# Optimization experiments

Hardware: AMD Instinct MI355X
Metric: run time of the kernel (lower is better)

Reference implementation:

```python
import jax, jax.numpy as jnp
import numpy as np

EPS = 1e-6  # nn.PairwiseDistance default eps (added to the difference)


def setup_inputs() -> dict:
    key = jax.random.key(0)
    feature = jax.random.normal(key, (16384, 256), dtype=jnp.float32)
    return {"feature": feature}


def reference(feature) -> jnp.ndarray:
    n = feature.shape[0]
    # all-pairs inner products [n, n]
    dots = jnp.matmul(feature, feature.T)
    # mask self-similarity on the diagonal with -1 (as in the torch code)
    dots = dots.at[jnp.diag_indices(n)].set(-1.0)
    # row-wise nearest neighbor (argmax of inner product)
    I = jnp.argmax(dots, axis=1)  # [n] int
    # PairwiseDistance(p=2): ||x1 - x2 + eps||_2
    diff = feature - feature[I] + EPS  # [n, d]
    distances = jnp.sqrt(jnp.sum(diff * diff, axis=1))  # [n]
    loss_uniform = -jnp.mean(jnp.log(n * distances))
    return loss_uniform
```

## Files before the change

### kernel.cpp

```cpp
#include <hip/hip_runtime.h>
#include <hip/hip_bf16.h>
#include <math.h>


#define NROWS 16384
#define DIM   256
#define BM    128
#define BN    128
#define EPSF  1e-6f

typedef __attribute__((ext_vector_type(4))) float f32x4;

typedef const __attribute__((address_space(1))) void* gas1_t;
typedef __attribute__((address_space(3))) void* las3_t;

__device__ __forceinline__ void glds16(const void* g, void* l) {
    __builtin_amdgcn_global_load_lds((gas1_t)g, (las3_t)l, 16, 0, 0);
}

__device__ __forceinline__ unsigned umax2(unsigned a, unsigned b) {
    return a > b ? a : b;
}

__device__ __forceinline__ unsigned f2e4m3(float f) {
    union { float f; unsigned u; } x; x.f = f;
    const unsigned s = (x.u >> 24) & 0x80u;
    const unsigned au = x.u & 0x7FFFFFFFu;
    float af = __uint_as_float(au);
    if (au < 0x3B800000u) {
        const int q = (int)(af * 512.0f + 0.5f);
        return s | (unsigned)q;
    }
    const unsigned add = 0x7FFFFu + ((au >> 20) & 1u);
    const unsigned v = au + add;
    const unsigned e = (v >> 23) - 120u;
    return s | (e << 3) | ((v >> 20) & 7u);
}

__global__ __launch_bounds__(256)
void convert_kernel(const float* __restrict__ F, unsigned char* __restrict__ F8,
                    unsigned long long* __restrict__ packed,
                    unsigned long long* __restrict__ scratch)
{
    const int t = blockIdx.x * 256 + threadIdx.x;
    const float4 a = *reinterpret_cast<const float4*>(F + (size_t)t * 8);
    const float4 b = *reinterpret_cast<const float4*>(F + (size_t)t * 8 + 4);
    const unsigned lo = f2e4m3(a.x) | (f2e4m3(a.y) << 8) |
                        (f2e4m3(a.z) << 16) | (f2e4m3(a.w) << 24);
    const unsigned hi = f2e4m3(b.x) | (f2e4m3(b.y) << 8) |
                        (f2e4m3(b.z) << 16) | (f2e4m3(b.w) << 24);
    uint2 v; v.x = lo; v.y = hi;
    *reinterpret_cast<uint2*>(F8 + (size_t)t * 8) = v;
    if (t < NROWS) packed[t] = 0ull;
    #pragma unroll
    for (int q = 0; q < 4; ++q)
        scratch[(size_t)t * 4 + q] = 0ull;
}

__global__ __launch_bounds__(256, 3)
void mfma_sym_fp8_kernel(const unsigned char* __restrict__ F8,
                         unsigned long long* __restrict__ packed,
                         unsigned long long* __restrict__ scratch)
{
    __shared__ __align__(16) unsigned char As[32768];
    __shared__ __align__(16) unsigned char Bs[2 * 8192];

    const int tid  = threadIdx.x;
    const int w    = tid >> 6;
    const int l    = tid & 63;
    const int rs   = (int)blockIdx.x >> 3;
    const int ck   = (int)blockIdx.x & 7;
    const int span = 128 - rs;
    const int t0   = rs + (span * ck) / 8;
    const int t1   = rs + (span * (ck + 1)) / 8;
    if (t0 >= t1) return;

    const int row0 = rs * BM;
    const int wrow = (w >> 1) * 64;
    const int wcol = (w & 1) * 64;
    const int lc   = l & 15;
    const int lr4  = l >> 4;

    #pragma unroll
    for (int m = 0; m < 8; ++m) {
        const int q   = 8 * w + m;
        const int k16 = q >> 1;
        const int row = (q & 1) * 64 + l;
        glds16(F8 + (size_t)(row0 + row) * DIM + k16 * 16, &As[q * 1024]);
    }

    #pragma unroll
    for (int q2 = 0; q2 < 2; ++q2) {
        const int col = q2 * 64 + l;
        glds16(F8 + (size_t)(t0 * BM + col) * DIM + w * 16,
               &Bs[(2 * w + q2) * 1024]);
    }

    const long* __restrict__ Al = reinterpret_cast<const long*>(As);

    f32x4 acc[4][4];
    #pragma unroll
    for (int i = 0; i < 4; ++i)
        #pragma unroll
        for (int j = 0; j < 4; ++j)
            acc[i][j] = (f32x4){512.f, 512.f, 512.f, 512.f};

    unsigned best[4][4] = {};

    const int k16r = (lr4 >> 1);
    const int odd  = lr4 & 1;

    for (int t = t0; t < t1; ++t) {
        const bool dt = (t == rs);
        #pragma unroll
        for (int ss = 0; ss < 4; ++ss) {
            __syncthreads();

            const int nt  = (ss < 3) ? t : t + 1;
            const int nss = (ss < 3) ? ss + 1 : 0;
            if (nt < t1) {
                #pragma unroll
                for (int q2 = 0; q2 < 2; ++q2) {
                    const int col = q2 * 64 + l;
                    glds16(F8 + (size_t)(nt * BM + col) * DIM + nss * 64 + w * 16,
                           &Bs[((ss & 1) ^ 1) * 8192 + (2 * w + q2) * 1024]);
                }
            }

            const long* __restrict__ Bl =
                reinterpret_cast<const long*>(Bs) + (ss & 1) * 1024;

            #pragma unroll
            for (int h = 0; h < 2; ++h) {
                const int kk = h * 2 + k16r;
                long afv[4], bfv[4];
                #pragma unroll
                for (int i = 0; i < 4; ++i) {
                    const int r = wrow + i * 16 + lc;
                    afv[i] = Al[(ss * 4 + kk) * 256 + r * 2 + odd];
                }
                #pragma unroll
                for (int j = 0; j < 4; ++j) {
                    const int c = wcol + j * 16 + lc;
                    bfv[j] = Bl[kk * 256 + c * 2 + odd];
                }
                #pragma unroll
                for (int j = 0; j < 4; ++j)
                    #pragma unroll
                    for (int i = 0; i < 4; ++i)
                        acc[i][j] = __builtin_amdgcn_mfma_f32_16x16x32_fp8_fp8(
                            afv[i], bfv[j], acc[i][j], 0, 0, 0);
            }
        }

        #pragma unroll
        for (int j = 0; j < 4; ++j) {
            unsigned kb = 0u;
            #pragma unroll
            for (int i = 0; i < 4; ++i)
                #pragma unroll
                for (int g = 0; g < 4; ++g) {
                    const int r_loc = wrow + i * 16 + lr4 * 4 + g;
                    unsigned key = (__float_as_uint(acc[i][j][g]) & 0xFFFFF800u)
                                   | (unsigned)(127 - r_loc);
                    if (dt && (wcol + j * 16 + lc == r_loc)) key = 0u;
                    kb = umax2(kb, key);
                }
            kb = umax2(kb, (unsigned)__shfl_xor((int)kb, 16));
            kb = umax2(kb, (unsigned)__shfl_xor((int)kb, 32));
            if (lr4 == 0) {
                const unsigned grow = (unsigned)row0 + (127u - (kb & 0x7FFu));
                const unsigned long long pk =
                    ((unsigned long long)(kb & 0xFFFFF800u) << 32) |
                    (0xFFFFFFFFu - grow);
                atomicMax(&scratch[((size_t)t * 128 + rs) * 128
                                   + wcol + j * 16 + lc], pk);
            }
        }

        const int tl = t - t0;
        unsigned cb[4];
        #pragma unroll
        for (int j = 0; j < 4; ++j)
            cb[j] = 2047u - (unsigned)(tl * 128 + wcol + j * 16 + lc);

        if (dt) {
            #pragma unroll
            for (int i = 0; i < 4; ++i)
                #pragma unroll
                for (int g = 0; g < 4; ++g) {
                    const int r_loc = wrow + i * 16 + lr4 * 4 + g;
                    unsigned bk = best[i][g];
                    #pragma unroll
                    for (int j = 0; j < 4; ++j) {
                        unsigned key = (__float_as_uint(acc[i][j][g])
                                        & 0xFFFFF800u) | cb[j];
                        if (wcol + j * 16 + lc == r_loc) key = 0u;
                        bk = umax2(bk, key);
                        acc[i][j][g] = 512.f;
                    }
                    best[i][g] = bk;
                }
        } else {
            #pragma unroll
            for (int i = 0; i < 4; ++i)
                #pragma unroll
                for (int g = 0; g < 4; ++g) {
                    const unsigned k0 = (__float_as_uint(acc[i][0][g]) & 0xFFFFF800u) | cb[0];
                    const unsigned k1 = (__float_as_uint(acc[i][1][g]) & 0xFFFFF800u) | cb[1];
                    const unsigned k2 = (__float_as_uint(acc[i][2][g]) & 0xFFFFF800u) | cb[2];
                    const unsigned k3 = (__float_as_uint(acc[i][3][g]) & 0xFFFFF800u) | cb[3];
                    best[i][g] = umax2(best[i][g],
                                       umax2(umax2(k0, k1), umax2(k2, k3)));
                    acc[i][0][g] = 512.f; acc[i][1][g] = 512.f;
                    acc[i][2][g] = 512.f; acc[i][3][g] = 512.f;
                }
        }
    }

    #pragma unroll
    for (int i = 0; i < 4; ++i)
        #pragma unroll
        for (int g = 0; g < 4; ++g) {
            unsigned key = best[i][g];
            #pragma unroll
            for (int m = 8; m >= 1; m >>= 1)
                key = umax2(key, (unsigned)__shfl_xor((int)key, m));
            if (lc == 0) {
                const int r = row0 + wrow + i * 16 + lr4 * 4 + g;
                const unsigned c = (unsigned)(t0 * BM) + (2047u - (key & 0x7FFu));
                const unsigned long long pk =
                    ((unsigned long long)(key & 0xFFFFF800u) << 32) |
                    (0xFFFFFFFFu - c);
                atomicMax(&packed[r], pk);
            }
        }
}

__global__ __launch_bounds__(256)
void dist_loss_kernel(const float* __restrict__ F,
                      const unsigned long long* __restrict__ packed,
                      const unsigned long long* __restrict__ scratch,
                      double* __restrict__ partials)
{
    const int tid  = threadIdx.x;
    const int lane = tid & 63;
    const int w    = tid >> 6;
    const int gw   = blockIdx.x * 4 + w;
    double local = 0.0;
    for (int r = gw; r < NROWS; r += 1024) {
        const int tR = r >> 7;
        const int cl = r & 127;
        unsigned long long best = packed[r];
        const unsigned long long* base = scratch + (size_t)tR * 16384 + cl;
        if (lane <= tR) {
            unsigned long long v = base[(size_t)lane * 128];
            if (lane + 64 <= tR) {
                const unsigned long long v2 = base[(size_t)(lane + 64) * 128];
                if (v2 > v) v = v2;
            }
            if (v > best) best = v;
        }
        #pragma unroll
        for (int m = 32; m >= 1; m >>= 1) {
            const unsigned long long o = __shfl_xor(best, m);
            if (o > best) best = o;
        }
        const int idx = (int)(0xFFFFFFFFu - (unsigned)(best & 0xFFFFFFFFull));

        const float4 a = *reinterpret_cast<const float4*>(
            F + (size_t)r * DIM + (lane << 2));
        const float4 b = *reinterpret_cast<const float4*>(
            F + (size_t)idx * DIM + (lane << 2));
        const float dx = a.x - b.x + EPSF;
        const float dy = a.y - b.y + EPSF;
        const float dz = a.z - b.z + EPSF;
        const float dw = a.w - b.w + EPSF;
        float ss = dx * dx + dy * dy + dz * dz + dw * dw;
        #pragma unroll
        for (int m = 32; m >= 1; m >>= 1) ss += __shfl_xor(ss, m);
        if (lane == 0)
            local += 0.5 * log((double)ss) + log((double)NROWS);
    }
    __shared__ double sm[4];
    if (lane == 0) sm[w] = local;
    __syncthreads();
    if (tid == 0) partials[blockIdx.x] = sm[0] + sm[1] + sm[2] + sm[3];
}

__global__ __launch_bounds__(256)
void finalize_kernel(const double* __restrict__ partials, float* __restrict__ out)
{
    const int tid = threadIdx.x;
    double v = partials[tid];
    #pragma unroll
    for (int m = 32; m >= 1; m >>= 1) v += __shfl_xor(v, m);
    __shared__ double sm[4];
    if ((tid & 63) == 0) sm[tid >> 6] = v;
    __syncthreads();
    if (tid == 0) out[0] = (float)(-(sm[0] + sm[1] + sm[2] + sm[3]) / (double)NROWS);
}

extern "C" void kernel_launch(void* const* d_in, const int* in_sizes, int n_in,
                              void* d_out, int out_size, void* d_ws, size_t ws_size,
                              hipStream_t stream)
{
    const float* F   = (const float*)d_in[0];
    float*       out = (float*)d_out;

    char* ws = (char*)d_ws;
    unsigned char*      F8       = (unsigned char*)ws;
    unsigned long long* packed   = (unsigned long long*)(ws + 4194304);
    unsigned long long* scratch  = (unsigned long long*)(ws + 4325376);
    double*             partials = (double*)(ws + 21102592);

    convert_kernel<<<2048, 256, 0, stream>>>(F, F8, packed, scratch);
    mfma_sym_fp8_kernel<<<(NROWS / BM) * 8, 256, 0, stream>>>(F8, packed, scratch);
    dist_loss_kernel<<<256, 256, 0, stream>>>(F, packed, scratch, partials);
    finalize_kernel<<<1, 256, 0, stream>>>(partials, out);
}
```

Measured before the change: 106.7 us.

## Pipeline B loads three stages deep and replace scratch atomics with plain stores

The B-tile pipeline moves from a double buffer with a full __syncthreads per 64-byte k-slice to a four-slot ring of 32-byte k-slices. Loads are issued three slices ahead, with explicit vmcnt waits and raw s_barrier. Column maxima are now combined across the two row-warps through shared memory and written to scratch with plain stores, so scratch no longer needs zeroing in the convert kernel. The block order is remapped so light and heavy triangular row strips are interleaved. The fp8 subnormal threshold is also changed, which may alter the rounding of small values.

```diff
diff --git a/kernel.cpp b/kernel.cpp
--- a/kernel.cpp
+++ b/kernel.cpp
@@ -5,8 +5,6 @@
 
 #define NROWS 16384
 #define DIM   256
-#define BM    128
-#define BN    128
 #define EPSF  1e-6f
 
 typedef __attribute__((ext_vector_type(4))) float f32x4;
@@ -26,8 +24,8 @@
     union { float f; unsigned u; } x; x.f = f;
     const unsigned s = (x.u >> 24) & 0x80u;
     const unsigned au = x.u & 0x7FFFFFFFu;
-    float af = __uint_as_float(au);
-    if (au < 0x3B800000u) {
+    const float af = __uint_as_float(au);
+    if (au < 0x3C800000u) {
         const int q = (int)(af * 512.0f + 0.5f);
         return s | (unsigned)q;
     }
@@ -39,8 +37,7 @@
 
 __global__ __launch_bounds__(256)
 void convert_kernel(const float* __restrict__ F, unsigned char* __restrict__ F8,
-                    unsigned long long* __restrict__ packed,
-                    unsigned long long* __restrict__ scratch)
+                    unsigned long long* __restrict__ packed)
 {
     const int t = blockIdx.x * 256 + threadIdx.x;
     const float4 a = *reinterpret_cast<const float4*>(F + (size_t)t * 8);
@@ -52,49 +49,51 @@
     uint2 v; v.x = lo; v.y = hi;
     *reinterpret_cast<uint2*>(F8 + (size_t)t * 8) = v;
     if (t < NROWS) packed[t] = 0ull;
-    #pragma unroll
-    for (int q = 0; q < 4; ++q)
-        scratch[(size_t)t * 4 + q] = 0ull;
 }
 
 __global__ __launch_bounds__(256, 3)
-void mfma_sym_fp8_kernel(const unsigned char* __restrict__ F8,
-                         unsigned long long* __restrict__ packed,
-                         unsigned long long* __restrict__ scratch)
+void mfma_sym_fp8_pipe(const unsigned char* __restrict__ F8,
+                       unsigned long long* __restrict__ packed,
+                       unsigned long long* __restrict__ scratch)
 {
     __shared__ __align__(16) unsigned char As[32768];
-    __shared__ __align__(16) unsigned char Bs[2 * 8192];
-
-    const int tid  = threadIdx.x;
-    const int w    = tid >> 6;
-    const int l    = tid & 63;
-    const int rs   = (int)blockIdx.x >> 3;
-    const int ck   = (int)blockIdx.x & 7;
+    __shared__ __align__(16) unsigned char Bs[16384];
+    __shared__ unsigned cmb[256];
+
+    const int tid = threadIdx.x;
+    const int w   = tid >> 6;
+    const int l   = tid & 63;
+
+    const int bid  = (int)blockIdx.x;
+    const int kgen = bid >> 8;
+    const int m5   = (bid >> 3) & 31;
+    const int ck   = bid & 7;
+    const int rs   = (kgen == 0) ? m5 :
+                     (kgen == 1) ? 63 - m5 :
+                     (kgen == 2) ? 64 + m5 : 127 - m5;
     const int span = 128 - rs;
-    const int t0   = rs + (span * ck) / 8;
-    const int t1   = rs + (span * (ck + 1)) / 8;
+    const int t0   = rs + ((span * ck) >> 3);
+    const int t1   = rs + ((span * (ck + 1)) >> 3);
     if (t0 >= t1) return;
 
-    const int row0 = rs * BM;
+    const int row0 = rs * 128;
     const int wrow = (w >> 1) * 64;
     const int wcol = (w & 1) * 64;
     const int lc   = l & 15;
     const int lr4  = l >> 4;
+    const int k16r = lr4 >> 1;
+    const int odd  = lr4 & 1;
 
     #pragma unroll
     for (int m = 0; m < 8; ++m) {
-        const int q   = 8 * w + m;
-        const int k16 = q >> 1;
-        const int row = (q & 1) * 64 + l;
-        glds16(F8 + (size_t)(row0 + row) * DIM + k16 * 16, &As[q * 1024]);
-    }
-
-    #pragma unroll
-    for (int q2 = 0; q2 < 2; ++q2) {
-        const int col = q2 * 64 + l;
-        glds16(F8 + (size_t)(t0 * BM + col) * DIM + w * 16,
-               &Bs[(2 * w + q2) * 1024]);
-    }
+        const int q = 8 * w + m;
+        glds16(F8 + (size_t)(row0 + (q & 1) * 64 + l) * DIM + (q >> 1) * 16,
+               &As[q * 1024]);
+    }
+    #pragma unroll
+    for (int sl = 0; sl < 3; ++sl)
+        glds16(F8 + (size_t)(t0 * 128 + (w & 1) * 64 + l) * DIM + sl * 32 + (w >> 1) * 16,
+               &Bs[sl * 4096 + w * 1024]);
 
     const long* __restrict__ Al = reinterpret_cast<const long*>(As);
 
@@ -107,51 +106,48 @@
 
     unsigned best[4][4] = {};
 
-    const int k16r = (lr4 >> 1);
-    const int odd  = lr4 & 1;
-
     for (int t = t0; t < t1; ++t) {
-        const bool dt = (t == rs);
-        #pragma unroll
-        for (int ss = 0; ss < 4; ++ss) {
-            __syncthreads();
-
-            const int nt  = (ss < 3) ? t : t + 1;
-            const int nss = (ss < 3) ? ss + 1 : 0;
-            if (nt < t1) {
+        const bool dt   = (t == rs);
+        const bool last = (t == t1 - 1);
+
+        #pragma unroll
+        for (int q = 0; q < 8; ++q) {
+            if (!last || q < 6)      asm volatile("s_waitcnt vmcnt(2)" ::: "memory");
+            else if (q == 6)         asm volatile("s_waitcnt vmcnt(1)" ::: "memory");
+            else                     asm volatile("s_waitcnt vmcnt(0)" ::: "memory");
+            __builtin_amdgcn_s_barrier();
+
+            if (!last || q < 5) {
+                const int nt = t + ((q + 3) >> 3);
+                const int nq = (q + 3) & 7;
+                glds16(F8 + (size_t)(nt * 128 + (w & 1) * 64 + l) * DIM
+                           + nq * 32 + (w >> 1) * 16,
+                       &Bs[((q + 3) & 3) * 4096 + w * 1024]);
+            }
+
+            const long* __restrict__ Bl =
+                reinterpret_cast<const long*>(Bs + (q & 3) * 4096);
+
+            long afv[4], bfv[4];
+            #pragma unroll
+            for (int i = 0; i < 4; ++i)
+                afv[i] = Al[(2 * q + k16r) * 256 + (wrow + i * 16 + lc) * 2 + odd];
+            #pragma unroll
+            for (int j = 0; j < 4; ++j)
+                bfv[j] = Bl[k16r * 256 + (wcol + j * 16 + lc) * 2 + odd];
+            #pragma unroll
+            for (int j = 0; j < 4; ++j)
                 #pragma unroll
-                for (int q2 = 0; q2 < 2; ++q2) {
-                    const int col = q2 * 64 + l;
-                    glds16(F8 + (size_t)(nt * BM + col) * DIM + nss * 64 + w * 16,
-                           &Bs[((ss & 1) ^ 1) * 8192 + (2 * w + q2) * 1024]);
-                }
-            }
-
-            const long* __restrict__ Bl =
-                reinterpret_cast<const long*>(Bs) + (ss & 1) * 1024;
-
-            #pragma unroll
-            for (int h = 0; h < 2; ++h) {
-                const int kk = h * 2 + k16r;
-                long afv[4], bfv[4];
-                #pragma unroll
-                for (int i = 0; i < 4; ++i) {
-                    const int r = wrow + i * 16 + lc;
-                    afv[i] = Al[(ss * 4 + kk) * 256 + r * 2 + odd];
-                }
-                #pragma unroll
-                for (int j = 0; j < 4; ++j) {
-                    const int c = wcol + j * 16 + lc;
-                    bfv[j] = Bl[kk * 256 + c * 2 + odd];
-                }
-                #pragma unroll
-                for (int j = 0; j < 4; ++j)
-                    #pragma unroll
-                    for (int i = 0; i < 4; ++i)
-                        acc[i][j] = __builtin_amdgcn_mfma_f32_16x16x32_fp8_fp8(
-                            afv[i], bfv[j], acc[i][j], 0, 0, 0);
-            }
-        }
+                for (int i = 0; i < 4; ++i)
+                    acc[i][j] = __builtin_amdgcn_mfma_f32_16x16x32_fp8_fp8(
+                        afv[i], bfv[j], acc[i][j], 0, 0, 0);
+        }
+
+        const int tl = t - t0;
+        unsigned cbA[4];
+        #pragma unroll
+        for (int j = 0; j < 4; ++j)
+            cbA[j] = 2047u - (unsigned)(tl * 128 + wcol + j * 16 + lc);
 
         #pragma unroll
         for (int j = 0; j < 4; ++j) {
@@ -161,60 +157,25 @@
                 #pragma unroll
                 for (int g = 0; g < 4; ++g) {
                     const int r_loc = wrow + i * 16 + lr4 * 4 + g;
-                    unsigned key = (__float_as_uint(acc[i][j][g]) & 0xFFFFF800u)
-                                   | (unsigned)(127 - r_loc);
-                    if (dt && (wcol + j * 16 + lc == r_loc)) key = 0u;
-                    kb = umax2(kb, key);
+                    unsigned m = __float_as_uint(acc[i][j][g]) & 0xFFFFF800u;
+                    if (dt && (wcol + j * 16 + lc == r_loc)) m = 0u;
+                    best[i][g] = umax2(best[i][g], m | cbA[j]);
+                    kb = umax2(kb, m | (unsigned)(127 - r_loc));
+                    acc[i][j][g] = 512.f;
                 }
             kb = umax2(kb, (unsigned)__shfl_xor((int)kb, 16));
             kb = umax2(kb, (unsigned)__shfl_xor((int)kb, 32));
-            if (lr4 == 0) {
-                const unsigned grow = (unsigned)row0 + (127u - (kb & 0x7FFu));
-                const unsigned long long pk =
-                    ((unsigned long long)(kb & 0xFFFFF800u) << 32) |
-                    (0xFFFFFFFFu - grow);
-                atomicMax(&scratch[((size_t)t * 128 + rs) * 128
-                                   + wcol + j * 16 + lc], pk);
-            }
-        }
-
-        const int tl = t - t0;
-        unsigned cb[4];
-        #pragma unroll
-        for (int j = 0; j < 4; ++j)
-            cb[j] = 2047u - (unsigned)(tl * 128 + wcol + j * 16 + lc);
-
-        if (dt) {
-            #pragma unroll
-            for (int i = 0; i < 4; ++i)
-                #pragma unroll
-                for (int g = 0; g < 4; ++g) {
-                    const int r_loc = wrow + i * 16 + lr4 * 4 + g;
-                    unsigned bk = best[i][g];
-                    #pragma unroll
-                    for (int j = 0; j < 4; ++j) {
-                        unsigned key = (__float_as_uint(acc[i][j][g])
-                                        & 0xFFFFF800u) | cb[j];
-                        if (wcol + j * 16 + lc == r_loc) key = 0u;
-                        bk = umax2(bk, key);
-                        acc[i][j][g] = 512.f;
-                    }
-                    best[i][g] = bk;
-                }
-        } else {
-            #pragma unroll
-            for (int i = 0; i < 4; ++i)
-                #pragma unroll
-                for (int g = 0; g < 4; ++g) {
-                    const unsigned k0 = (__float_as_uint(acc[i][0][g]) & 0xFFFFF800u) | cb[0];
-                    const unsigned k1 = (__float_as_uint(acc[i][1][g]) & 0xFFFFF800u) | cb[1];
-                    const unsigned k2 = (__float_as_uint(acc[i][2][g]) & 0xFFFFF800u) | cb[2];
-                    const unsigned k3 = (__float_as_uint(acc[i][3][g]) & 0xFFFFF800u) | cb[3];
-                    best[i][g] = umax2(best[i][g],
-                                       umax2(umax2(k0, k1), umax2(k2, k3)));
-                    acc[i][0][g] = 512.f; acc[i][1][g] = 512.f;
-                    acc[i][2][g] = 512.f; acc[i][3][g] = 512.f;
-                }
+            if (lr4 == 0) cmb[(w >> 1) * 128 + wcol + j * 16 + lc] = kb;
+        }
+        asm volatile("s_waitcnt lgkmcnt(0)" ::: "memory");
+        __builtin_amdgcn_s_barrier();
+        if (w < 2) {
+            const int c = w * 64 + l;
+            const unsigned km = umax2(cmb[c], cmb[128 + c]);
+            const unsigned grow = (unsigned)row0 + (127u - (km & 0x7FFu));
+            scratch[((size_t)t * 128 + rs) * 128 + c] =
+                ((unsigned long long)(km & 0xFFFFF800u) << 32) |
+                (0xFFFFFFFFu - grow);
         }
     }
 
@@ -228,11 +189,10 @@
                 key = umax2(key, (unsigned)__shfl_xor((int)key, m));
             if (lc == 0) {
                 const int r = row0 + wrow + i * 16 + lr4 * 4 + g;
-                const unsigned c = (unsigned)(t0 * BM) + (2047u - (key & 0x7FFu));
-                const unsigned long long pk =
-                    ((unsigned long long)(key & 0xFFFFF800u) << 32) |
-                    (0xFFFFFFFFu - c);
-                atomicMax(&packed[r], pk);
+                const unsigned c = (unsigned)(t0 * 128) + (2047u - (key & 0x7FFu));
+                atomicMax(&packed[r],
+                          ((unsigned long long)(key & 0xFFFFF800u) << 32) |
+                          (0xFFFFFFFFu - c));
             }
         }
 }
@@ -314,8 +274,8 @@
     unsigned long long* scratch  = (unsigned long long*)(ws + 4325376);
     double*             partials = (double*)(ws + 21102592);
 
-    convert_kernel<<<2048, 256, 0, stream>>>(F, F8, packed, scratch);
-    mfma_sym_fp8_kernel<<<(NROWS / BM) * 8, 256, 0, stream>>>(F8, packed, scratch);
+    convert_kernel<<<2048, 256, 0, stream>>>(F, F8, packed);
+    mfma_sym_fp8_pipe<<<1024, 256, 0, stream>>>(F8, packed, scratch);
     dist_loss_kernel<<<256, 256, 0, stream>>>(F, packed, scratch, partials);
     finalize_kernel<<<1, 256, 0, stream>>>(partials, out);
 }
```

Measured after the change: 110.3 us. 1.03x slower.
